# Optimization experiments

Measured on AMD Instinct MI355X. Metric: run time of the kernel, lower is better.

Reference implementation:

```python
import jax, jax.numpy as jnp
import numpy as np

N_T = 50000   # target cells
N_S = 100000  # source cells
E = 400000    # nonzeros per sparse operator
IN_CH = 128
OUT_CH = 256
N_MLP = 3     # Linear+ReLU layers per branch (1 + mlp_hidden)


def setup_inputs() -> dict:
    key = jax.random.key(0)
    ks = jax.random.split(key, 20)
    s_in = (2.0 / (IN_CH + OUT_CH)) ** 0.5
    s_hid = (2.0 / (OUT_CH + OUT_CH)) ** 0.5
    s_m = (2.0 / (2 * OUT_CH + OUT_CH)) ** 0.5
    return {
        "x_target": jax.random.normal(ks[0], (N_T, OUT_CH), jnp.float32),
        "x_src0": jax.random.normal(ks[1], (N_S, IN_CH), jnp.float32),
        "x_src1": jax.random.normal(ks[2], (N_S, IN_CH), jnp.float32),
        "vals0": jax.random.normal(ks[3], (E,), jnp.float32),
        "vals1": jax.random.normal(ks[4], (E,), jnp.float32),
        "rows0": jax.random.randint(ks[5], (E,), 0, N_T, jnp.int32),
        "cols0": jax.random.randint(ks[6], (E,), 0, N_S, jnp.int32),
        "rows1": jax.random.randint(ks[7], (E,), 0, N_T, jnp.int32),
        "cols1": jax.random.randint(ks[8], (E,), 0, N_S, jnp.int32),
        "W0": jax.random.normal(ks[9], (IN_CH, OUT_CH), jnp.float32) * s_in,
        "W1": jax.random.normal(ks[10], (IN_CH, OUT_CH), jnp.float32) * s_in,
        "mlp_W0": jax.random.normal(ks[11], (N_MLP, OUT_CH, OUT_CH), jnp.float32) * s_hid,
        "mlp_b0": jnp.zeros((N_MLP, OUT_CH), jnp.float32),
        "mlp_W1": jax.random.normal(ks[12], (N_MLP, OUT_CH, OUT_CH), jnp.float32) * s_hid,
        "mlp_b1": jnp.zeros((N_MLP, OUT_CH), jnp.float32),
        "Wm": jax.random.normal(ks[13], (2 * OUT_CH, OUT_CH), jnp.float32) * s_m,
        "bm": jnp.zeros((OUT_CH,), jnp.float32),
    }


def _branch(x_target, x_src, rows, cols, vals, W, mlp_W, mlp_b, epsilon=0.0):
    # support = x_source @ weight  (channel dims differ)
    support = x_src @ W                                   # [N_S, OUT]
    # propagate: sparse A @ support via gather + segment_sum (signed values kept)
    msgs = vals[:, None] * support[cols]                  # [E, OUT]
    agg = jax.ops.segment_sum(msgs, rows, num_segments=x_target.shape[0])
    h = agg + (1.0 + epsilon) * x_target                  # epsilon residual
    for i in range(N_MLP):                                # Linear -> ReLU, x3
        h = jax.nn.relu(h @ mlp_W[i] + mlp_b[i])
    return h


def reference(x_target, x_src0, x_src1, vals0, vals1, rows0, cols0, rows1, cols1,
              W0, W1, mlp_W0, mlp_b0, mlp_W1, mlp_b1, Wm, bm):
    h0 = _branch(x_target, x_src0, rows0, cols0, vals0, W0, mlp_W0, mlp_b0)
    h1 = _branch(x_target, x_src1, rows1, cols1, vals1, W1, mlp_W1, mlp_b1)
    # merge_type == 'conc': concat along channels then Linear
    return jnp.concatenate([h0, h1], axis=1) @ Wm + bm
```

## Files before the change

### kernel.cpp

```cpp
#include <hip/hip_runtime.h>
#include <stdint.h>

#define NT 50000
#define NS 100000
#define NE 400000
#define CIN 128
#define COUT 256

typedef unsigned short u16;
typedef short bf8 __attribute__((ext_vector_type(8)));
typedef float f4 __attribute__((ext_vector_type(4)));

__device__ __forceinline__ float bf2f(u16 u) {
  union { unsigned int i; float f; } x; x.i = ((unsigned int)u) << 16; return x.f;
}
__device__ __forceinline__ u16 f2bf(float f) {
  union { float f; unsigned int i; } x; x.f = f;
  return (u16)((x.i + 0x7fffu + ((x.i >> 16) & 1u)) >> 16);
}
__device__ __forceinline__ float loadf(const void* base, size_t eoff, int f32) {
  if (f32) return ((const float*)base)[eoff];
  return bf2f(((const u16*)base)[eoff]);
}

struct DetectArgs { const unsigned int* p[13]; int nw[13]; };

__global__ void detect_all(DetectArgs a, int* __restrict__ flags) {
  __shared__ int s_sane, s_nz;
  const int bi = blockIdx.x;
  const unsigned int* buf = a.p[bi];
  const int nw = a.nw[bi];
  if (threadIdx.x == 0) { s_sane = 0; s_nz = 0; }
  __syncthreads();
  int sane = 0, nz = 0;
  for (int i = threadIdx.x; i < nw; i += 256) {
    unsigned int w = buf[i];
    if (w != 0u) {
      ++nz;
      unsigned int e = (w >> 23) & 0xFFu;
      if (e >= 100u && e <= 140u) ++sane;
    }
  }
  atomicAdd(&s_sane, sane);
  atomicAdd(&s_nz, nz);
  __syncthreads();
  if (threadIdx.x == 0) flags[bi] = (s_nz > 0 && 2 * s_sane > s_nz) ? 1 : 0;
}

__global__ void convert_bf16(const void* __restrict__ src, const int* __restrict__ flag,
                             u16* __restrict__ dst, int n) {
  int t = (blockIdx.x * 256 + threadIdx.x) * 4;
  if (t >= n) return;
  if (*flag) {
    const float* s = (const float*)src + t;
    ushort4 o;
    o.x = f2bf(s[0]); o.y = f2bf(s[1]); o.z = f2bf(s[2]); o.w = f2bf(s[3]);
    *(ushort4*)&dst[t] = o;
  } else {
    *(ushort4*)&dst[t] = *(const ushort4*)((const u16*)src + t);
  }
}

__global__ void transpose_w(const void* __restrict__ src, const int* __restrict__ flag,
                            u16* __restrict__ dst, int K, int N, int total) {
  int t = blockIdx.x * 256 + threadIdx.x;
  if (t >= total) return;
  int f32 = *flag;
  int kn = K * N;
  int mat = t / kn, i = t - mat * kn;
  int n = i / K, k = i - n * K;
  size_t s = (size_t)mat * kn + (size_t)k * N + n;
  dst[t] = f32 ? f2bf(((const float*)src)[s]) : ((const u16*)src)[s];
}

template <bool RELU, bool BIAS, bool ACCUM, bool ADDMAT>
__global__ __launch_bounds__(256)
void gemm_bf16(const u16* __restrict__ A, int lda,
               const u16* __restrict__ Bt, int ldb,
               const u16* __restrict__ bias,
               const void* __restrict__ X, const int* __restrict__ xflag,
               void* __restrict__ C, int ldc, const int* __restrict__ outflag,
               int M, int K) {
  __shared__ __align__(16) u16 lA[128 * 32];
  __shared__ __align__(16) u16 lB[128 * 32];

  const int tid  = threadIdx.x;
  const int wave = tid >> 6;
  const int lane = tid & 63;
  const int m0 = blockIdx.x * 128;
  const int n0 = blockIdx.y * 128;
  const int wm = (wave >> 1) * 64;
  const int wn = (wave & 1) * 64;

  f4 acc[4][4];
#pragma unroll
  for (int i = 0; i < 4; ++i)
#pragma unroll
    for (int j = 0; j < 4; ++j) acc[i][j] = (f4){0.f, 0.f, 0.f, 0.f};

  const int r0 = tid >> 2;
  const int c0 = (tid & 3) * 8;
  int gr0 = m0 + r0;       if (gr0 >= M) gr0 = M - 1;
  int gr1 = m0 + r0 + 64;  if (gr1 >= M) gr1 = M - 1;
  const u16* a0 = A + (size_t)gr0 * lda + c0;
  const u16* a1 = A + (size_t)gr1 * lda + c0;
  const u16* b0 = Bt + (size_t)(n0 + r0) * ldb + c0;
  const u16* b1 = Bt + (size_t)(n0 + r0 + 64) * ldb + c0;

  const int krow = (lane >> 4) * 8;
  const int mrow = lane & 15;

  for (int k0 = 0; k0 < K; k0 += 32) {
    bf8 va0 = *(const bf8*)(a0 + k0);
    bf8 va1 = *(const bf8*)(a1 + k0);
    bf8 vb0 = *(const bf8*)(b0 + k0);
    bf8 vb1 = *(const bf8*)(b1 + k0);
    *(bf8*)&lA[tid * 8]        = va0;
    *(bf8*)&lA[2048 + tid * 8] = va1;
    *(bf8*)&lB[tid * 8]        = vb0;
    *(bf8*)&lB[2048 + tid * 8] = vb1;
    __syncthreads();

    bf8 aF[4], bF[4];
#pragma unroll
    for (int i = 0; i < 4; ++i)
      aF[i] = *(const bf8*)&lA[(wm + i * 16 + mrow) * 32 + krow];
#pragma unroll
    for (int j = 0; j < 4; ++j)
      bF[j] = *(const bf8*)&lB[(wn + j * 16 + mrow) * 32 + krow];

#pragma unroll
    for (int i = 0; i < 4; ++i)
#pragma unroll
      for (int j = 0; j < 4; ++j)
        acc[i][j] = __builtin_amdgcn_mfma_f32_16x16x32_bf16(aF[i], bF[j], acc[i][j], 0, 0, 0);
    __syncthreads();
  }

  const int xf = (ADDMAT && xflag) ? *xflag : 0;
  const int of = outflag ? *outflag : 0;
  const int crow = m0 + wm + (lane >> 4) * 4;
  const int ccol = n0 + wn + (lane & 15);
#pragma unroll
  for (int j = 0; j < 4; ++j) {
    const int col = ccol + j * 16;
    float bv = 0.f;
    if (BIAS) bv = bf2f(bias[col]);
#pragma unroll
    for (int i = 0; i < 4; ++i) {
      const int row = crow + i * 16;
#pragma unroll
      for (int r = 0; r < 4; ++r) {
        const int rr = row + r;
        if (rr < M) {
          const size_t idx = (size_t)rr * ldc + col;
          float v = acc[i][j][r] + bv;
          if (ADDMAT) v += loadf(X, idx, xf);
          if (of) {
            float* Cf = (float*)C;
            if (ACCUM) v += Cf[idx];
            if (RELU) v = fmaxf(v, 0.f);
            Cf[idx] = v;
          } else {
            u16* Cb = (u16*)C;
            if (ACCUM) v += bf2f(Cb[idx]);
            if (RELU) v = fmaxf(v, 0.f);
            Cb[idx] = f2bf(v);
          }
        }
      }
    }
  }
}

__global__ void hist_kernel(const int* __restrict__ rows0, const int* __restrict__ rows1,
                            int* __restrict__ cnt) {
  int t = blockIdx.x * 256 + threadIdx.x;
  if (t >= 2 * NE) return;
  int seg = (t < NE) ? rows0[t] : (NT + rows1[t - NE]);
  atomicAdd(&cnt[seg], 1);
}

__global__ void scanA(const int* __restrict__ cnt, int* __restrict__ incl,
                      int* __restrict__ bsum, int n) {
  __shared__ int sd[256];
  int t = threadIdx.x, g = blockIdx.x * 256 + t;
  int v = (g < n) ? cnt[g] : 0;
  sd[t] = v; __syncthreads();
  for (int o = 1; o < 256; o <<= 1) {
    int x = (t >= o) ? sd[t - o] : 0;
    __syncthreads();
    sd[t] += x;
    __syncthreads();
  }
  if (g < n) incl[g] = sd[t];
  if (t == 255) bsum[blockIdx.x] = sd[255];
}

__global__ void scanB(int* __restrict__ bsum, int nb) {
  __shared__ int sd[512];
  int t = threadIdx.x;
  int v = (t < nb) ? bsum[t] : 0;
  sd[t] = v; __syncthreads();
  for (int o = 1; o < 512; o <<= 1) {
    int x = (t >= o) ? sd[t - o] : 0;
    __syncthreads();
    sd[t] += x;
    __syncthreads();
  }
  if (t < nb) bsum[t] = sd[t] - v;
}

__global__ void scanC(const int* __restrict__ cnt, const int* __restrict__ incl,
                      const int* __restrict__ bsum, int* __restrict__ row_ptr,
                      int n, int total) {
  int g = blockIdx.x * 256 + threadIdx.x;
  if (g == 0) row_ptr[n] = total;
  if (g >= n) return;
  row_ptr[g] = incl[g] - cnt[g] + bsum[blockIdx.x];
}

__global__ void scatter_kernel(const int* __restrict__ rows0, const int* __restrict__ cols0,
                               const void* __restrict__ vals0, const int* __restrict__ v0f,
                               const int* __restrict__ rows1, const int* __restrict__ cols1,
                               const void* __restrict__ vals1, const int* __restrict__ v1f,
                               const int* __restrict__ row_ptr, int* __restrict__ cnt,
                               int* __restrict__ scol, float* __restrict__ sval) {
  int t = blockIdx.x * 256 + threadIdx.x;
  if (t >= 2 * NE) return;
  int seg, col; float v;
  if (t < NE) { seg = rows0[t]; col = cols0[t]; v = loadf(vals0, t, *v0f); }
  else { int e = t - NE; seg = NT + rows1[e]; col = cols1[e]; v = loadf(vals1, e, *v1f); }
  int pos = row_ptr[seg] + atomicAdd(&cnt[seg], 1);
  scol[pos] = col;
  sval[pos] = v;
}

__global__ __launch_bounds__(256)
void spmm_gather(const int* __restrict__ row_ptr, const int* __restrict__ scol,
                 const float* __restrict__ sval, const u16* __restrict__ Xs,
                 u16* __restrict__ agg, int seg_base) {
  int wid = blockIdx.x * 4 + (threadIdx.x >> 6);
  int lane = threadIdx.x & 63;
  if (wid >= NT) return;
  int seg = seg_base + wid;
  int p0 = row_ptr[seg], p1 = row_ptr[seg + 1];
  int c = lane * 2;
  float a0 = 0.f, a1 = 0.f;
  int p = p0;
  for (; p + 3 < p1; p += 4) {
    int c0 = scol[p], c1 = scol[p + 1], c2 = scol[p + 2], c3 = scol[p + 3];
    float v0 = sval[p], v1 = sval[p + 1], v2 = sval[p + 2], v3 = sval[p + 3];
    ushort2 s0 = *(const ushort2*)&Xs[(size_t)c0 * CIN + c];
    ushort2 s1 = *(const ushort2*)&Xs[(size_t)c1 * CIN + c];
    ushort2 s2 = *(const ushort2*)&Xs[(size_t)c2 * CIN + c];
    ushort2 s3 = *(const ushort2*)&Xs[(size_t)c3 * CIN + c];
    a0 += v0 * bf2f(s0.x); a1 += v0 * bf2f(s0.y);
    a0 += v1 * bf2f(s1.x); a1 += v1 * bf2f(s1.y);
    a0 += v2 * bf2f(s2.x); a1 += v2 * bf2f(s2.y);
    a0 += v3 * bf2f(s3.x); a1 += v3 * bf2f(s3.y);
  }
  for (; p < p1; ++p) {
    int cc = scol[p];
    float v = sval[p];
    ushort2 s = *(const ushort2*)&Xs[(size_t)cc * CIN + c];
    a0 += v * bf2f(s.x); a1 += v * bf2f(s.y);
  }
  ushort2 o;
  o.x = f2bf(a0); o.y = f2bf(a1);
  *(ushort2*)&agg[(size_t)wid * CIN + c] = o;
}

extern "C" void kernel_launch(void* const* d_in, const int* in_sizes, int n_in,
                              void* d_out, int out_size, void* d_ws, size_t ws_size,
                              hipStream_t stream) {
  (void)n_in; (void)out_size; (void)ws_size;

  int I_xt, I_xs0, I_xs1, I_v0, I_v1, I_r0, I_c0, I_r1, I_c1,
      I_W0, I_W1, I_mW0, I_mb0, I_mW1, I_mb1, I_Wm, I_bm;
  if (in_sizes[0] == 32768) {
    I_W0 = 0; I_W1 = 1; I_Wm = 2; I_bm = 3; I_c0 = 4; I_c1 = 5;
    I_mW0 = 6; I_mW1 = 7; I_mb0 = 8; I_mb1 = 9; I_r0 = 10; I_r1 = 11;
    I_v0 = 12; I_v1 = 13; I_xs0 = 14; I_xs1 = 15; I_xt = 16;
  } else {
    I_xt = 0; I_xs0 = 1; I_xs1 = 2; I_v0 = 3; I_v1 = 4; I_r0 = 5; I_c0 = 6;
    I_r1 = 7; I_c1 = 8; I_W0 = 9; I_W1 = 10; I_mW0 = 11; I_mb0 = 12;
    I_mW1 = 13; I_mb1 = 14; I_Wm = 15; I_bm = 16;
  }
  const void* x_target = d_in[I_xt];
  const void* x_src0   = d_in[I_xs0];
  const void* x_src1   = d_in[I_xs1];
  const void* vals0    = d_in[I_v0];
  const void* vals1    = d_in[I_v1];
  const int* rows0     = (const int*)d_in[I_r0];
  const int* cols0     = (const int*)d_in[I_c0];
  const int* rows1     = (const int*)d_in[I_r1];
  const int* cols1     = (const int*)d_in[I_c1];
  const void* W0       = d_in[I_W0];
  const void* W1       = d_in[I_W1];
  const void* mW0      = d_in[I_mW0];
  const void* mb0      = d_in[I_mb0];
  const void* mW1      = d_in[I_mW1];
  const void* mb1      = d_in[I_mb1];
  const void* Wm       = d_in[I_Wm];
  const void* bm       = d_in[I_bm];

  char* ws = (char*)d_ws;
  size_t off = 0;
  auto alloc = [&](size_t bytes) -> char* {
    off = (off + 255) & ~(size_t)255;
    char* p = ws + off;
    off += bytes;
    return p;
  };
  int* flags = (int*)alloc(16 * 4);
  u16* W0t   = (u16*)alloc((size_t)COUT * CIN * 2);
  u16* W1t   = (u16*)alloc((size_t)COUT * CIN * 2);
  u16* mW0t  = (u16*)alloc((size_t)3 * COUT * COUT * 2);
  u16* mW1t  = (u16*)alloc((size_t)3 * COUT * COUT * 2);
  u16* Wmt   = (u16*)alloc((size_t)COUT * 512 * 2);
  u16* mbc   = (u16*)alloc((size_t)2 * 3 * COUT * 2);
  u16* bmc   = (u16*)alloc((size_t)COUT * 2);
  u16* xsc   = (u16*)alloc((size_t)NS * CIN * 2);
  u16* agg   = (u16*)alloc((size_t)NT * CIN * 2);
  u16* hA    = (u16*)alloc((size_t)NT * COUT * 2);
  u16* hB    = (u16*)alloc((size_t)NT * COUT * 2);
  int* cnt     = (int*)alloc((size_t)2 * NT * 4);
  int* row_ptr = (int*)alloc(((size_t)2 * NT + 1) * 4);
  int* incl    = (int*)alloc((size_t)2 * NT * 4);
  int* bsum    = (int*)alloc(512 * 4);
  int* scol    = (int*)alloc((size_t)2 * NE * 4);
  float* sval  = (float*)alloc((size_t)2 * NE * 4);

  DetectArgs da;
  const void* dp[13]  = {x_target, x_src0, x_src1, vals0, vals1, W0, W1,
                         mW0, mb0, mW1, mb1, Wm, bm};
  const int   dn[13]  = {NT * COUT, NS * CIN, NS * CIN, NE, NE,
                         CIN * COUT, CIN * COUT, 3 * COUT * COUT, 3 * COUT,
                         3 * COUT * COUT, 3 * COUT, 512 * COUT, COUT};
  for (int i = 0; i < 13; ++i) {
    da.p[i] = (const unsigned int*)dp[i];
    int nw = dn[i] / 2; if (nw > 8192) nw = 8192; if (nw < 1) nw = 1;
    da.nw[i] = nw;
  }
  detect_all<<<13, 256, 0, stream>>>(da, flags);

  transpose_w<<<(CIN * COUT + 255) / 256, 256, 0, stream>>>(W0, flags + 5, W0t, CIN, COUT, CIN * COUT);
  transpose_w<<<(CIN * COUT + 255) / 256, 256, 0, stream>>>(W1, flags + 6, W1t, CIN, COUT, CIN * COUT);
  transpose_w<<<(3 * COUT * COUT + 255) / 256, 256, 0, stream>>>(mW0, flags + 7, mW0t, COUT, COUT, 3 * COUT * COUT);
  transpose_w<<<(3 * COUT * COUT + 255) / 256, 256, 0, stream>>>(mW1, flags + 9, mW1t, COUT, COUT, 3 * COUT * COUT);
  transpose_w<<<(512 * COUT + 255) / 256, 256, 0, stream>>>(Wm, flags + 11, Wmt, 512, COUT, 512 * COUT);
  convert_bf16<<<1, 256, 0, stream>>>(mb0, flags + 8,  mbc,            3 * COUT);
  convert_bf16<<<1, 256, 0, stream>>>(mb1, flags + 10, mbc + 3 * COUT, 3 * COUT);
  convert_bf16<<<1, 256, 0, stream>>>(bm,  flags + 12, bmc,            COUT);

  hipMemsetAsync(cnt, 0, (size_t)2 * NT * 4, stream);
  hist_kernel<<<(2 * NE + 255) / 256, 256, 0, stream>>>(rows0, rows1, cnt);
  const int nseg = 2 * NT;
  const int nb = (nseg + 255) / 256;
  scanA<<<nb, 256, 0, stream>>>(cnt, incl, bsum, nseg);
  scanB<<<1, 512, 0, stream>>>(bsum, nb);
  scanC<<<nb, 256, 0, stream>>>(cnt, incl, bsum, row_ptr, nseg, 2 * NE);
  hipMemsetAsync(cnt, 0, (size_t)2 * NT * 4, stream);
  scatter_kernel<<<(2 * NE + 255) / 256, 256, 0, stream>>>(
      rows0, cols0, vals0, flags + 3, rows1, cols1, vals1, flags + 4,
      row_ptr, cnt, scol, sval);

  dim3 gm((NT + 127) / 128, 2);
  for (int b = 0; b < 2; ++b) {
    const void* xs = b ? x_src1 : x_src0;
    const int* xsf = flags + (b ? 2 : 1);
    const u16* Wt  = b ? W1t : W0t;
    const u16* mWt = b ? mW1t : mW0t;
    const u16* mb  = mbc + b * 3 * COUT;

    convert_bf16<<<(NS * CIN / 4 + 255) / 256, 256, 0, stream>>>(xs, xsf, xsc, NS * CIN);
    spmm_gather<<<NT / 4, 256, 0, stream>>>(row_ptr, scol, sval, xsc, agg, b * NT);
    gemm_bf16<false, false, false, true><<<gm, 256, 0, stream>>>(
        agg, CIN, Wt, CIN, nullptr, x_target, flags + 0, hA, COUT, nullptr, NT, CIN);
    gemm_bf16<true, true, false, false><<<gm, 256, 0, stream>>>(
        hA, COUT, mWt, COUT, mb, nullptr, nullptr, hB, COUT, nullptr, NT, COUT);
    gemm_bf16<true, true, false, false><<<gm, 256, 0, stream>>>(
        hB, COUT, mWt + COUT * COUT, COUT, mb + COUT, nullptr, nullptr, hA, COUT, nullptr, NT, COUT);
    gemm_bf16<true, true, false, false><<<gm, 256, 0, stream>>>(
        hA, COUT, mWt + 2 * COUT * COUT, COUT, mb + 2 * COUT, nullptr, nullptr, hB, COUT, nullptr, NT, COUT);
    if (b == 0) {
      gemm_bf16<false, true, false, false><<<gm, 256, 0, stream>>>(
          hB, COUT, Wmt, 512, bmc, nullptr, nullptr, d_out, COUT, flags + 0, NT, COUT);
    } else {
      gemm_bf16<false, false, true, false><<<gm, 256, 0, stream>>>(
          hB, COUT, Wmt + COUT, 512, nullptr, nullptr, nullptr, d_out, COUT, flags + 0, NT, COUT);
    }
  }
}
```

Measured before the change: 763.0 us.

## Drop LDS staging in GEMM, load MFMA fragments directly with register double-buffering

```diff
diff --git a/kernel.cpp b/kernel.cpp
--- a/kernel.cpp
+++ b/kernel.cpp
@@ -81,16 +81,25 @@
                const void* __restrict__ X, const int* __restrict__ xflag,
                void* __restrict__ C, int ldc, const int* __restrict__ outflag,
                int M, int K) {
-  __shared__ __align__(16) u16 lA[128 * 32];
-  __shared__ __align__(16) u16 lB[128 * 32];
-
   const int tid  = threadIdx.x;
   const int wave = tid >> 6;
   const int lane = tid & 63;
-  const int m0 = blockIdx.x * 128;
-  const int n0 = blockIdx.y * 128;
-  const int wm = (wave >> 1) * 64;
-  const int wn = (wave & 1) * 64;
+  const int m0 = blockIdx.x * 64;
+  const int wn = wave * 64;
+  const int mrow = lane & 15;
+  const int krow = (lane >> 4) * 8;
+
+  const u16* ap[4];
+  const u16* bp[4];
+#pragma unroll
+  for (int i = 0; i < 4; ++i) {
+    int r = m0 + i * 16 + mrow;
+    if (r >= M) r = M - 1;
+    ap[i] = A + (size_t)r * lda + krow;
+  }
+#pragma unroll
+  for (int j = 0; j < 4; ++j)
+    bp[j] = Bt + (size_t)(wn + j * 16 + mrow) * ldb + krow;
 
   f4 acc[4][4];
 #pragma unroll
@@ -98,49 +107,37 @@
 #pragma unroll
     for (int j = 0; j < 4; ++j) acc[i][j] = (f4){0.f, 0.f, 0.f, 0.f};
 
-  const int r0 = tid >> 2;
-  const int c0 = (tid & 3) * 8;
-  int gr0 = m0 + r0;       if (gr0 >= M) gr0 = M - 1;
-  int gr1 = m0 + r0 + 64;  if (gr1 >= M) gr1 = M - 1;
-  const u16* a0 = A + (size_t)gr0 * lda + c0;
-  const u16* a1 = A + (size_t)gr1 * lda + c0;
-  const u16* b0 = Bt + (size_t)(n0 + r0) * ldb + c0;
-  const u16* b1 = Bt + (size_t)(n0 + r0 + 64) * ldb + c0;
-
-  const int krow = (lane >> 4) * 8;
-  const int mrow = lane & 15;
-
-  for (int k0 = 0; k0 < K; k0 += 32) {
-    bf8 va0 = *(const bf8*)(a0 + k0);
-    bf8 va1 = *(const bf8*)(a1 + k0);
-    bf8 vb0 = *(const bf8*)(b0 + k0);
-    bf8 vb1 = *(const bf8*)(b1 + k0);
-    *(bf8*)&lA[tid * 8]        = va0;
-    *(bf8*)&lA[2048 + tid * 8] = va1;
-    *(bf8*)&lB[tid * 8]        = vb0;
-    *(bf8*)&lB[2048 + tid * 8] = vb1;
-    __syncthreads();
-
-    bf8 aF[4], bF[4];
+  auto loadf8 = [&](bf8* av, bf8* bv, int kk) {
+#pragma unroll
+    for (int i = 0; i < 4; ++i) av[i] = *(const bf8*)(ap[i] + kk);
+#pragma unroll
+    for (int j = 0; j < 4; ++j) bv[j] = *(const bf8*)(bp[j] + kk);
+  };
+  auto mfmas = [&](const bf8* av, const bf8* bv) {
 #pragma unroll
     for (int i = 0; i < 4; ++i)
-      aF[i] = *(const bf8*)&lA[(wm + i * 16 + mrow) * 32 + krow];
-#pragma unroll
-    for (int j = 0; j < 4; ++j)
-      bF[j] = *(const bf8*)&lB[(wn + j * 16 + mrow) * 32 + krow];
-
-#pragma unroll
-    for (int i = 0; i < 4; ++i)
 #pragma unroll
       for (int j = 0; j < 4; ++j)
-        acc[i][j] = __builtin_amdgcn_mfma_f32_16x16x32_bf16(aF[i], bF[j], acc[i][j], 0, 0, 0);
-    __syncthreads();
-  }
+        acc[i][j] = __builtin_amdgcn_mfma_f32_16x16x32_bf16(av[i], bv[j], acc[i][j], 0, 0, 0);
+  };
+
+  bf8 a0[4], b0[4], a1[4], b1[4];
+  loadf8(a0, b0, 0);
+  int k0 = 32;
+  for (; k0 + 32 < K; k0 += 64) {
+    loadf8(a1, b1, k0);
+    mfmas(a0, b0);
+    loadf8(a0, b0, k0 + 32);
+    mfmas(a1, b1);
+  }
+  loadf8(a1, b1, K - 32);
+  mfmas(a0, b0);
+  mfmas(a1, b1);
 
   const int xf = (ADDMAT && xflag) ? *xflag : 0;
   const int of = outflag ? *outflag : 0;
-  const int crow = m0 + wm + (lane >> 4) * 4;
-  const int ccol = n0 + wn + (lane & 15);
+  const int crow = m0 + (lane >> 4) * 4;
+  const int ccol = wn + (lane & 15);
 #pragma unroll
   for (int j = 0; j < 4; ++j) {
     const int col = ccol + j * 16;
@@ -366,7 +363,7 @@
       rows0, cols0, vals0, flags + 3, rows1, cols1, vals1, flags + 4,
       row_ptr, cnt, scol, sval);
 
-  dim3 gm((NT + 127) / 128, 2);
+  dim3 gm((NT + 63) / 64);
   for (int b = 0; b < 2; ++b) {
     const void* xs = b ? x_src1 : x_src0;
     const int* xsf = flags + (b ? 2 : 1);
```

New measurement: 857.9 us. +12.4%, slower.
